# Performance work log

Hardware: AMD Instinct MI355X
Metric: run time of the kernel (lower is better)

The kernel has to match this reference:

```python
import jax, jax.numpy as jnp
import numpy as np

N = 40000; E = 640000; F_IN = 128; HID = 32; HEADS = 4; G = 64
NEG_SLOPE = 0.2; LN_EPS = 1e-5


def setup_inputs() -> dict:
    key = jax.random.key(0)
    ks = jax.random.split(key, 24)
    rn = lambda k, shape, s=0.1: jax.random.normal(k, shape, jnp.float32) * s
    d = {}
    d["x"] = jax.random.normal(ks[0], (N, F_IN), jnp.float32)
    d["edge_index"] = jax.random.randint(ks[1], (2, E), 0, N)
    d["batch"] = jnp.sort(jax.random.randint(ks[2], (N,), 0, G))
    # GAT layer 0: in F_IN -> HID per head, HEADS heads, concat
    d["W0"] = rn(ks[3], (F_IN, HEADS * HID))
    d["as0"] = rn(ks[4], (HEADS, HID)); d["ad0"] = rn(ks[5], (HEADS, HID))
    d["b0"] = jnp.zeros((HEADS * HID,), jnp.float32)
    d["ln0_g"] = jnp.ones((HEADS * HID,), jnp.float32); d["ln0_b"] = jnp.zeros((HEADS * HID,), jnp.float32)
    # GAT layer 1: HEADS*HID -> HID per head, HEADS heads, concat
    d["W1"] = rn(ks[6], (HEADS * HID, HEADS * HID))
    d["as1"] = rn(ks[7], (HEADS, HID)); d["ad1"] = rn(ks[8], (HEADS, HID))
    d["b1"] = jnp.zeros((HEADS * HID,), jnp.float32)
    d["ln1_g"] = jnp.ones((HEADS * HID,), jnp.float32); d["ln1_b"] = jnp.zeros((HEADS * HID,), jnp.float32)
    # GAT layer 2: HEADS*HID -> HID, 1 head, no concat
    d["W2"] = rn(ks[9], (HEADS * HID, HID))
    d["as2"] = rn(ks[10], (1, HID)); d["ad2"] = rn(ks[11], (1, HID))
    d["b2"] = jnp.zeros((HID,), jnp.float32)
    d["ln2_g"] = jnp.ones((HID,), jnp.float32); d["ln2_b"] = jnp.zeros((HID,), jnp.float32)
    # classifier: HID -> HID//2 -> 2
    d["fc1_w"] = rn(ks[12], (HID, HID // 2)); d["fc1_b"] = jnp.zeros((HID // 2,), jnp.float32)
    d["fc2_w"] = rn(ks[13], (HID // 2, 2)); d["fc2_b"] = jnp.zeros((2,), jnp.float32)
    return d


def gat_layer(x, src, dst, W, a_s, a_d, b, heads, out_c, concat):
    n = x.shape[0]
    h = (x @ W).reshape(n, heads, out_c)            # [N,H,C]
    al_s = jnp.sum(h * a_s, axis=-1)                # [N,H]
    al_d = jnp.sum(h * a_d, axis=-1)                # [N,H]
    e = jax.nn.leaky_relu(al_s[src] + al_d[dst], NEG_SLOPE)  # [E,H]
    m = jax.ops.segment_max(e, dst, num_segments=n)          # segment softmax over dst
    ex = jnp.exp(e - m[dst])
    s = jax.ops.segment_sum(ex, dst, num_segments=n)
    alpha = ex / (s[dst] + 1e-16)                   # [E,H]
    out = jax.ops.segment_sum(h[src] * alpha[:, :, None], dst, num_segments=n)  # [N,H,C]
    out = out.reshape(n, heads * out_c) if concat else out.mean(axis=1)
    return out + b


def layer_norm(x, g, b):
    mu = x.mean(-1, keepdims=True)
    var = jnp.var(x, axis=-1, keepdims=True)
    return (x - mu) * jax.lax.rsqrt(var + LN_EPS) * g + b


def reference(x, edge_index, batch, W0, as0, ad0, b0, ln0_g, ln0_b, W1, as1, ad1, b1, ln1_g, ln1_b, W2, as2, ad2, b2, ln2_g, ln2_b, fc1_w, fc1_b, fc2_w, fc2_b):
    src, dst = edge_index[0], edge_index[1]
    h = gat_layer(x, src, dst, W0, as0, ad0, b0, HEADS, HID, True)
    h = jax.nn.elu(layer_norm(h, ln0_g, ln0_b))
    h = gat_layer(h, src, dst, W1, as1, ad1, b1, HEADS, HID, True)
    h = jax.nn.elu(layer_norm(h, ln1_g, ln1_b))
    h = gat_layer(h, src, dst, W2, as2, ad2, b2, 1, HID, False)
    h = jax.nn.elu(layer_norm(h, ln2_g, ln2_b))
    cnt = jax.ops.segment_sum(jnp.ones((h.shape[0],), h.dtype), batch, num_segments=G)
    hg = jax.ops.segment_sum(h, batch, num_segments=G) / jnp.maximum(cnt, 1.0)[:, None]  # global mean pool [G,HID]
    z = jax.nn.relu(hg @ fc1_w + fc1_b)
    return z @ fc2_w + fc2_b
```

## Files before the change

kernel.cpp:

```cpp
#include <hip/hip_runtime.h>
#include <hip/hip_fp16.h>
#include <math.h>

#define NN 40000
#define EE 640000
#define NG 64
#define SCAN_BLOCKS ((NN + 1023) / 1024)

__device__ __forceinline__ float eluf(float x) { return x > 0.f ? x : expm1f(x); }

typedef const __attribute__((address_space(1))) char gas_char;
typedef __attribute__((address_space(3))) char las_char;

__device__ __forceinline__ void async_copy16(void* l, const void* g) {
  __builtin_amdgcn_global_load_lds((gas_char*)g, (las_char*)l, 16, 0, 0);
}

typedef __fp16 f16x2 __attribute__((ext_vector_type(2)));
__device__ __forceinline__ unsigned packh(float lo, float hi) {
  f16x2 p = __builtin_amdgcn_cvt_pkrtz(lo, hi);
  union { f16x2 h; unsigned u; } c; c.h = p; return c.u;
}
__device__ __forceinline__ float hlo(unsigned p) {
  union { unsigned u; f16x2 h; } c; c.u = p; return (float)c.h.x;
}
__device__ __forceinline__ float hhi(unsigned p) {
  union { unsigned u; f16x2 h; } c; c.u = p; return (float)c.h.y;
}
__device__ __forceinline__ float h16f(unsigned short u) {
  union { unsigned u32; f16x2 h; } c; c.u32 = u; return (float)c.h.x;
}

__global__ void zero_int_kernel(int* __restrict__ p, int n) {
  int i = blockIdx.x * 256 + threadIdx.x;
  if (i < n) p[i] = 0;
}

__global__ void count_deg_kernel(const int* __restrict__ dst, int* __restrict__ deg, int e) {
  int i0 = (blockIdx.x * 256 + threadIdx.x) * 4;
  if (i0 + 4 <= e) {
    int4 d4 = *reinterpret_cast<const int4*>(&dst[i0]);
    atomicAdd(&deg[d4.x], 1);
    atomicAdd(&deg[d4.y], 1);
    atomicAdd(&deg[d4.z], 1);
    atomicAdd(&deg[d4.w], 1);
  } else {
    for (int i = i0; i < e; ++i) atomicAdd(&deg[dst[i]], 1);
  }
}

__global__ __launch_bounds__(1024) void scanA_kernel(const int* __restrict__ deg,
                                                     int* __restrict__ row_ptr,
                                                     int* __restrict__ bsum, int n) {
  __shared__ int wsum[16];
  int t = threadIdx.x, lane = t & 63, wid = t >> 6;
  int i = blockIdx.x * 1024 + t;
  int v = (i < n) ? deg[i] : 0;
#pragma unroll
  for (int off = 1; off < 64; off <<= 1) {
    int u = __shfl_up(v, off);
    if (lane >= off) v += u;
  }
  if (lane == 63) wsum[wid] = v;
  __syncthreads();
  if (t < 16) {
    int w = wsum[t];
#pragma unroll
    for (int off = 1; off < 16; off <<= 1) {
      int u = __shfl_up(w, off);
      if (t >= off) w += u;
    }
    wsum[t] = w;
  }
  __syncthreads();
  if (wid > 0) v += wsum[wid - 1];
  if (i < n) row_ptr[i + 1] = v;
  if (t == 1023) bsum[blockIdx.x] = v;
}

__global__ __launch_bounds__(1024) void scanC_kernel(int* __restrict__ row_ptr,
                                                     const int* __restrict__ bsum,
                                                     int* __restrict__ cursor, int n) {
  __shared__ int off_s;
  int t = threadIdx.x;
  int b = blockIdx.x;
  if (t < 64) {
    int v = (t < b && t < SCAN_BLOCKS) ? bsum[t] : 0;
#pragma unroll
    for (int m = 1; m < 64; m <<= 1) v += __shfl_xor(v, m);
    if (t == 0) off_s = v;
  }
  __syncthreads();
  int off = off_s;
  int i = b * 1024 + t;
  if (i < n) {
    int v = row_ptr[i + 1] + off;
    row_ptr[i + 1] = v;
    if (i + 1 < n) cursor[i + 1] = v;
    if (i == 0) { cursor[0] = 0; row_ptr[0] = 0; }
  }
}

__global__ void scatter_kernel(const int* __restrict__ src, const int* __restrict__ dst,
                               int* __restrict__ cursor, int* __restrict__ csr_src, int e) {
  int i0 = (blockIdx.x * 256 + threadIdx.x) * 4;
  if (i0 + 4 <= e) {
    int4 s4 = *reinterpret_cast<const int4*>(&src[i0]);
    int4 d4 = *reinterpret_cast<const int4*>(&dst[i0]);
    int p0 = atomicAdd(&cursor[d4.x], 1);
    int p1 = atomicAdd(&cursor[d4.y], 1);
    int p2 = atomicAdd(&cursor[d4.z], 1);
    int p3 = atomicAdd(&cursor[d4.w], 1);
    csr_src[p0] = s4.x;
    csr_src[p1] = s4.y;
    csr_src[p2] = s4.z;
    csr_src[p3] = s4.w;
  } else {
    for (int i = i0; i < e; ++i) {
      int d = dst[i];
      int pos = atomicAdd(&cursor[d], 1);
      csr_src[pos] = src[i];
    }
  }
}

__global__ __launch_bounds__(256, 3) void gemm128_kernel(
    const float* __restrict__ x, const float* __restrict__ W,
    const float* __restrict__ a_s, const float* __restrict__ a_d,
    unsigned* __restrict__ hb, float* __restrict__ als, float* __restrict__ ald)
{
  __shared__ float xs[2][64 * 32];
  __shared__ float ws[2][32 * 128];

  int t = threadIdx.x;
  int row0 = blockIdx.x * 64;
  const char* xgb = (const char*)x + (size_t)row0 * 512;

  {
    int li0 = t, li1 = t + 256;
    async_copy16((char*)xs[0] + li0 * 16, xgb + (li0 >> 3) * 512 + (li0 & 7) * 16);
    async_copy16((char*)xs[0] + li1 * 16, xgb + (li1 >> 3) * 512 + (li1 & 7) * 16);
    const char* wg = (const char*)W;
#pragma unroll
    for (int p = 0; p < 4; ++p)
      async_copy16((char*)ws[0] + p * 4096 + t * 16, wg + p * 4096 + t * 16);
  }
  __syncthreads();

  int cg = t & 31, rg = t >> 5;
  int r0 = rg * 8;
  int jlo = 2 * cg;

  float acc[8][4];
#pragma unroll
  for (int r = 0; r < 8; ++r)
#pragma unroll
    for (int c = 0; c < 4; ++c) acc[r][c] = 0.f;

  for (int ch = 0; ch < 4; ++ch) {
    if (ch < 3) {
      int b = (ch + 1) & 1;
      int li0 = t, li1 = t + 256;
      const char* xg = xgb + (ch + 1) * 128;
      async_copy16((char*)xs[b] + li0 * 16, xg + (li0 >> 3) * 512 + (li0 & 7) * 16);
      async_copy16((char*)xs[b] + li1 * 16, xg + (li1 >> 3) * 512 + (li1 & 7) * 16);
      const char* wg = (const char*)W + (size_t)(ch + 1) * 32 * 128 * 4;
#pragma unroll
      for (int p = 0; p < 4; ++p)
        async_copy16((char*)ws[b] + p * 4096 + t * 16, wg + p * 4096 + t * 16);
    }
    const float* wc = ws[ch & 1];
    const float* xc = xs[ch & 1];
#pragma unroll
    for (int kk = 0; kk < 32; kk += 4) {
      float2 wlo[4], whi[4];
#pragma unroll
      for (int q = 0; q < 4; ++q) {
        wlo[q] = *reinterpret_cast<const float2*>(&wc[(kk + q) * 128 + jlo]);
        whi[q] = *reinterpret_cast<const float2*>(&wc[(kk + q) * 128 + 64 + jlo]);
      }
#pragma unroll
      for (int r = 0; r < 8; ++r) {
        float4 xv = *reinterpret_cast<const float4*>(&xc[(r0 + r) * 32 + kk]);
        float a0 = acc[r][0], a1 = acc[r][1], a2 = acc[r][2], a3 = acc[r][3];
        a0 = fmaf(xv.x, wlo[0].x, a0); a1 = fmaf(xv.x, wlo[0].y, a1);
        a2 = fmaf(xv.x, whi[0].x, a2); a3 = fmaf(xv.x, whi[0].y, a3);
        a0 = fmaf(xv.y, wlo[1].x, a0); a1 = fmaf(xv.y, wlo[1].y, a1);
        a2 = fmaf(xv.y, whi[1].x, a2); a3 = fmaf(xv.y, whi[1].y, a3);
        a0 = fmaf(xv.z, wlo[2].x, a0); a1 = fmaf(xv.z, wlo[2].y, a1);
        a2 = fmaf(xv.z, whi[2].x, a2); a3 = fmaf(xv.z, whi[2].y, a3);
        a0 = fmaf(xv.w, wlo[3].x, a0); a1 = fmaf(xv.w, wlo[3].y, a1);
        a2 = fmaf(xv.w, whi[3].x, a2); a3 = fmaf(xv.w, whi[3].y, a3);
        acc[r][0] = a0; acc[r][1] = a1; acc[r][2] = a2; acc[r][3] = a3;
      }
    }
    __syncthreads();
  }

#pragma unroll
  for (int r = 0; r < 8; ++r) {
    uint2 pv;
    pv.x = packh(acc[r][0], acc[r][2]);
    pv.y = packh(acc[r][1], acc[r][3]);
    *reinterpret_cast<uint2*>(&hb[(size_t)(row0 + r0 + r) * 64 + jlo]) = pv;
  }

  float as0 = a_s[jlo], as1 = a_s[jlo + 1], as2 = a_s[jlo + 64], as3 = a_s[jlo + 65];
  float ad0 = a_d[jlo], ad1 = a_d[jlo + 1], ad2 = a_d[jlo + 64], ad3 = a_d[jlo + 65];
  int lane = t & 63;
#pragma unroll
  for (int r = 0; r < 8; ++r) {
    float psa = fmaf(acc[r][0], as0, acc[r][1] * as1);
    float psb = fmaf(acc[r][2], as2, acc[r][3] * as3);
    float pda = fmaf(acc[r][0], ad0, acc[r][1] * ad1);
    float pdb = fmaf(acc[r][2], ad2, acc[r][3] * ad3);
#pragma unroll
    for (int m = 1; m < 16; m <<= 1) {
      psa += __shfl_xor(psa, m); psb += __shfl_xor(psb, m);
      pda += __shfl_xor(pda, m); pdb += __shfl_xor(pdb, m);
    }
    if ((lane & 15) == 0) {
      int hA = (lane >> 4) & 1;
      size_t row = (size_t)(row0 + r0 + r);
      als[row * 4 + hA] = psa; als[row * 4 + hA + 2] = psb;
      ald[row * 4 + hA] = pda; ald[row * 4 + hA + 2] = pdb;
    }
  }
}

template<bool FUSE>
__global__ __launch_bounds__(256) void aggregate128_kernel(
    const unsigned* __restrict__ hb, const float* __restrict__ als, const float* __restrict__ ald,
    const int* __restrict__ row_ptr, const int* __restrict__ csr_src,
    const float* __restrict__ bias, const float* __restrict__ ln_g, const float* __restrict__ ln_b,
    float* __restrict__ out,
    const float* __restrict__ W2, const float* __restrict__ as2, const float* __restrict__ ad2,
    unsigned short* __restrict__ h2h, float* __restrict__ als2, float* __restrict__ ald2)
{
  __shared__ int s_src[4][2][32];
  __shared__ float2 s_w[4][2][32][2];
  __shared__ __align__(16) float w2s[FUSE ? 32 * 128 : 4];
  __shared__ __align__(16) float y_s[FUSE ? 8 * 128 : 4];

  int t = threadIdx.x, lane = t & 63, wid = t >> 6;
  int hw = lane >> 5, c = lane & 31;
  int node = blockIdx.x * 8 + wid * 2 + hw;

  if constexpr (FUSE) {
#pragma unroll
    for (int p = 0; p < 4; ++p)
      async_copy16((char*)w2s + p * 4096 + t * 16, (const char*)W2 + p * 4096 + t * 16);
    __syncthreads();
  }

  int start = row_ptr[node], end = row_ptr[node + 1];
  int deg = end - start;

  float4 adq = reinterpret_cast<const float4*>(ald)[node];
  int hsel = c >> 4;
  float a0 = 0.f, a1 = 0.f, a2 = 0.f, a3 = 0.f;
  float ssum0 = 0.f, ssum1 = 0.f;

  if (deg <= 32) {
    int s = 0;
    float ex0 = 0.f, ex1 = 0.f, ex2 = 0.f, ex3 = 0.f;
    if (c < deg) {
      s = csr_src[start + c];
      float4 q = reinterpret_cast<const float4*>(als)[s];
      float v0 = q.x + adq.x, v1 = q.y + adq.y, v2 = q.z + adq.z, v3 = q.w + adq.w;
      v0 = v0 > 0.f ? v0 : 0.2f * v0; v1 = v1 > 0.f ? v1 : 0.2f * v1;
      v2 = v2 > 0.f ? v2 : 0.2f * v2; v3 = v3 > 0.f ? v3 : 0.2f * v3;
      ex0 = __expf(v0); ex1 = __expf(v1); ex2 = __expf(v2); ex3 = __expf(v3);
    }
    s_src[wid][hw][c] = s;
    s_w[wid][hw][c][0] = make_float2(ex0, ex2);
    s_w[wid][hw][c][1] = make_float2(ex1, ex3);

    float b0a = 0.f, b1a = 0.f, b2a = 0.f, b3a = 0.f;
    float sb0 = 0.f, sb1 = 0.f;
    int j = 0;
    for (; j + 2 <= deg; j += 2) {
      int sa = s_src[wid][hw][j];
      int sb = s_src[wid][hw][j + 1];
      uint2 ua = *reinterpret_cast<const uint2*>(&hb[(size_t)sa * 64 + 2 * c]);
      uint2 ub = *reinterpret_cast<const uint2*>(&hb[(size_t)sb * 64 + 2 * c]);
      float2 wa = s_w[wid][hw][j][hsel];
      float2 wb = s_w[wid][hw][j + 1][hsel];
      a0 = fmaf(wa.x, hlo(ua.x), a0); a1 = fmaf(wa.x, hlo(ua.y), a1);
      a2 = fmaf(wa.y, hhi(ua.x), a2); a3 = fmaf(wa.y, hhi(ua.y), a3);
      ssum0 += wa.x; ssum1 += wa.y;
      b0a = fmaf(wb.x, hlo(ub.x), b0a); b1a = fmaf(wb.x, hlo(ub.y), b1a);
      b2a = fmaf(wb.y, hhi(ub.x), b2a); b3a = fmaf(wb.y, hhi(ub.y), b3a);
      sb0 += wb.x; sb1 += wb.y;
    }
    if (j < deg) {
      int sa = s_src[wid][hw][j];
      uint2 ua = *reinterpret_cast<const uint2*>(&hb[(size_t)sa * 64 + 2 * c]);
      float2 wa = s_w[wid][hw][j][hsel];
      a0 = fmaf(wa.x, hlo(ua.x), a0); a1 = fmaf(wa.x, hlo(ua.y), a1);
      a2 = fmaf(wa.y, hhi(ua.x), a2); a3 = fmaf(wa.y, hhi(ua.y), a3);
      ssum0 += wa.x; ssum1 += wa.y;
    }
    a0 += b0a; a1 += b1a; a2 += b2a; a3 += b3a;
    ssum0 += sb0; ssum1 += sb1;
  } else {
    for (int eb = 0; eb < deg; eb += 32) {
      int s = 0;
      float ex0 = 0.f, ex1 = 0.f, ex2 = 0.f, ex3 = 0.f;
      if (eb + c < deg) {
        s = csr_src[start + eb + c];
        float4 q = reinterpret_cast<const float4*>(als)[s];
        float v0 = q.x + adq.x, v1 = q.y + adq.y, v2 = q.z + adq.z, v3 = q.w + adq.w;
        v0 = v0 > 0.f ? v0 : 0.2f * v0; v1 = v1 > 0.f ? v1 : 0.2f * v1;
        v2 = v2 > 0.f ? v2 : 0.2f * v2; v3 = v3 > 0.f ? v3 : 0.2f * v3;
        ex0 = __expf(v0); ex1 = __expf(v1); ex2 = __expf(v2); ex3 = __expf(v3);
      }
      s_src[wid][hw][c] = s;
      s_w[wid][hw][c][0] = make_float2(ex0, ex2);
      s_w[wid][hw][c][1] = make_float2(ex1, ex3);
      int cnt = deg - eb; if (cnt > 32) cnt = 32;
      for (int j = 0; j < cnt; ++j) {
        int sj = s_src[wid][hw][j];
        uint2 u = *reinterpret_cast<const uint2*>(&hb[(size_t)sj * 64 + 2 * c]);
        float2 w = s_w[wid][hw][j][hsel];
        a0 = fmaf(w.x, hlo(u.x), a0); a1 = fmaf(w.x, hlo(u.y), a1);
        a2 = fmaf(w.y, hhi(u.x), a2); a3 = fmaf(w.y, hhi(u.y), a3);
        ssum0 += w.x; ssum1 += w.y;
      }
    }
  }

  float2 blo = *reinterpret_cast<const float2*>(&bias[2 * c]);
  float2 bhi = *reinterpret_cast<const float2*>(&bias[2 * c + 64]);
  float is0 = 1.f / (ssum0 + 1e-16f), is1 = 1.f / (ssum1 + 1e-16f);
  float o0 = a0 * is0 + blo.x;
  float o1 = a1 * is0 + blo.y;
  float o2 = a2 * is1 + bhi.x;
  float o3 = a3 * is1 + bhi.y;
  float red = o0 + o1 + o2 + o3;
  float sq2 = o0 * o0 + o1 * o1 + o2 * o2 + o3 * o3;
#pragma unroll
  for (int m = 1; m < 32; m <<= 1) {
    red += __shfl_xor(red, m);
    sq2 += __shfl_xor(sq2, m);
  }
  float mu = red * (1.f / 128.f);
  float var = sq2 * (1.f / 128.f) - mu * mu;
  float rstd = rsqrtf(var + 1e-5f);
  float2 glo = *reinterpret_cast<const float2*>(&ln_g[2 * c]);
  float2 ghi = *reinterpret_cast<const float2*>(&ln_g[2 * c + 64]);
  float2 bl2 = *reinterpret_cast<const float2*>(&ln_b[2 * c]);
  float2 bh2 = *reinterpret_cast<const float2*>(&ln_b[2 * c + 64]);
  float2 ylo, yhi;
  ylo.x = eluf((o0 - mu) * rstd * glo.x + bl2.x);
  ylo.y = eluf((o1 - mu) * rstd * glo.y + bl2.y);
  yhi.x = eluf((o2 - mu) * rstd * ghi.x + bh2.x);
  yhi.y = eluf((o3 - mu) * rstd * ghi.y + bh2.y);

  if constexpr (!FUSE) {
    *reinterpret_cast<float2*>(&out[(size_t)node * 128 + 2 * c]) = ylo;
    *reinterpret_cast<float2*>(&out[(size_t)node * 128 + 64 + 2 * c]) = yhi;
  } else {
    int nidx = (wid * 2 + hw) * 128;
    *reinterpret_cast<float2*>(&y_s[nidx + 2 * c]) = ylo;
    *reinterpret_cast<float2*>(&y_s[nidx + 64 + 2 * c]) = yhi;
    float ac0 = 0.f, ac1 = 0.f, ac2 = 0.f, ac3 = 0.f;
#pragma unroll
    for (int k = 0; k < 128; k += 4) {
      float4 yv = *reinterpret_cast<const float4*>(&y_s[nidx + k]);
      ac0 = fmaf(yv.x, w2s[(k + 0) * 32 + c], ac0);
      ac1 = fmaf(yv.y, w2s[(k + 1) * 32 + c], ac1);
      ac2 = fmaf(yv.z, w2s[(k + 2) * 32 + c], ac2);
      ac3 = fmaf(yv.w, w2s[(k + 3) * 32 + c], ac3);
    }
    float acc = (ac0 + ac1) + (ac2 + ac3);
    h2h[(size_t)node * 32 + c] = (unsigned short)(packh(acc, acc) & 0xffffu);
    float ps = acc * as2[c], pd = acc * ad2[c];
#pragma unroll
    for (int m = 1; m < 32; m <<= 1) { ps += __shfl_xor(ps, m); pd += __shfl_xor(pd, m); }
    if (c == 0) { als2[node] = ps; ald2[node] = pd; }
  }
}

__global__ __launch_bounds__(256) void aggregate32_kernel(
    const unsigned short* __restrict__ h, const float* __restrict__ als, const float* __restrict__ ald,
    const int* __restrict__ row_ptr, const int* __restrict__ csr_src,
    const float* __restrict__ bias, const float* __restrict__ ln_g, const float* __restrict__ ln_b,
    float* __restrict__ out, int n)
{
  __shared__ int s_src[4][2][32];
  __shared__ float s_ex[4][2][32];
  int t = threadIdx.x, lane = t & 63, wid = t >> 6;
  int hw = lane >> 5, c = lane & 31;
  int node = blockIdx.x * 8 + wid * 2 + hw;
  int start = row_ptr[node], end = row_ptr[node + 1];
  int deg = end - start;
  float adl = ald[node];
  float acc0 = 0.f, ssum = 0.f;

  if (deg <= 32) {
    int s = 0; float ex = 0.f;
    if (c < deg) {
      s = csr_src[start + c];
      float v = als[s] + adl;
      v = v > 0.f ? v : 0.2f * v;
      ex = __expf(v);
    }
    s_src[wid][hw][c] = s;
    s_ex[wid][hw][c] = ex;

    float acc1 = 0.f, ssum1 = 0.f;
    int j = 0;
    for (; j + 2 <= deg; j += 2) {
      int sa = s_src[wid][hw][j];
      int sb = s_src[wid][hw][j + 1];
      float ha = h16f(h[(size_t)sa * 32 + c]);
      float hbv = h16f(h[(size_t)sb * 32 + c]);
      float wa = s_ex[wid][hw][j];
      float wb = s_ex[wid][hw][j + 1];
      acc0 = fmaf(wa, ha, acc0); ssum += wa;
      acc1 = fmaf(wb, hbv, acc1); ssum1 += wb;
    }
    if (j < deg) {
      float wa = s_ex[wid][hw][j];
      acc0 = fmaf(wa, h16f(h[(size_t)s_src[wid][hw][j] * 32 + c]), acc0);
      ssum += wa;
    }
    acc0 += acc1; ssum += ssum1;
  } else {
    for (int eb = 0; eb < deg; eb += 32) {
      int s = 0; float ex = 0.f;
      if (eb + c < deg) {
        s = csr_src[start + eb + c];
        float v = als[s] + adl;
        v = v > 0.f ? v : 0.2f * v;
        ex = __expf(v);
      }
      s_src[wid][hw][c] = s;
      s_ex[wid][hw][c] = ex;
      int cnt = deg - eb; if (cnt > 32) cnt = 32;
      for (int j = 0; j < cnt; ++j) {
        float w = s_ex[wid][hw][j];
        acc0 = fmaf(w, h16f(h[(size_t)s_src[wid][hw][j] * 32 + c]), acc0);
        ssum += w;
      }
    }
  }

  float o0 = acc0 / (ssum + 1e-16f) + bias[c];
  float red = o0, sq2 = o0 * o0;
#pragma unroll
  for (int m = 1; m < 32; m <<= 1) {
    red += __shfl_xor(red, m);
    sq2 += __shfl_xor(sq2, m);
  }
  float mu = red * (1.f / 32.f);
  float var = sq2 * (1.f / 32.f) - mu * mu;
  float rstd = rsqrtf(var + 1e-5f);
  float y0 = (o0 - mu) * rstd * ln_g[c] + ln_b[c];
  out[(size_t)node * 32 + c] = eluf(y0);
}

__device__ __forceinline__ int lower_bound_dev(const int* a, int n, int key) {
  int lo = 0, hi = n;
  while (lo < hi) { int mid = (lo + hi) >> 1; if (a[mid] < key) lo = mid + 1; else hi = mid; }
  return lo;
}

__global__ __launch_bounds__(256) void poolfc_kernel(
    const float* __restrict__ x2, const int* __restrict__ batch,
    const float* __restrict__ fc1w, const float* __restrict__ fc1b,
    const float* __restrict__ fc2w, const float* __restrict__ fc2b,
    float* __restrict__ out, int n)
{
  int g = blockIdx.x;
  int lo = lower_bound_dev(batch, n, g);
  int hi = lower_bound_dev(batch, n, g + 1);
  int t = threadIdx.x;
  int c = t & 31, r = t >> 5;
  float acc = 0.f;
  for (int i = lo + r; i < hi; i += 8) acc += x2[(size_t)i * 32 + c];
  __shared__ float red[8][32];
  __shared__ float hgl[32];
  __shared__ float zl[16];
  red[r][c] = acc;
  __syncthreads();
  if (r == 0) {
    float s = 0.f;
#pragma unroll
    for (int k = 0; k < 8; ++k) s += red[k][c];
    float cnt = (float)(hi - lo);
    hgl[c] = s / fmaxf(cnt, 1.f);
  }
  __syncthreads();
  if (t < 16) {
    float a = fc1b[t];
#pragma unroll
    for (int k = 0; k < 32; ++k) a = fmaf(hgl[k], fc1w[k * 16 + t], a);
    zl[t] = fmaxf(a, 0.f);
  }
  __syncthreads();
  if (t < 2) {
    float a = fc2b[t];
#pragma unroll
    for (int j = 0; j < 16; ++j) a = fmaf(zl[j], fc2w[j * 2 + t], a);
    out[g * 2 + t] = a;
  }
}

extern "C" void kernel_launch(void* const* d_in, const int* in_sizes, int n_in,
                              void* d_out, int out_size, void* d_ws, size_t ws_size,
                              hipStream_t stream) {
  const float* x    = (const float*)d_in[0];
  const int*   ei   = (const int*)d_in[1];
  const int*   batch= (const int*)d_in[2];
  const float* W0   = (const float*)d_in[3];
  const float* as0  = (const float*)d_in[4];
  const float* ad0  = (const float*)d_in[5];
  const float* b0   = (const float*)d_in[6];
  const float* ln0g = (const float*)d_in[7];
  const float* ln0b = (const float*)d_in[8];
  const float* W1   = (const float*)d_in[9];
  const float* as1  = (const float*)d_in[10];
  const float* ad1  = (const float*)d_in[11];
  const float* b1   = (const float*)d_in[12];
  const float* ln1g = (const float*)d_in[13];
  const float* ln1b = (const float*)d_in[14];
  const float* W2   = (const float*)d_in[15];
  const float* as2  = (const float*)d_in[16];
  const float* ad2  = (const float*)d_in[17];
  const float* b2   = (const float*)d_in[18];
  const float* ln2g = (const float*)d_in[19];
  const float* ln2b = (const float*)d_in[20];
  const float* fc1w = (const float*)d_in[21];
  const float* fc1b = (const float*)d_in[22];
  const float* fc2w = (const float*)d_in[23];
  const float* fc2b = (const float*)d_in[24];
  float* out = (float*)d_out;

  const int* srce = ei;
  const int* dste = ei + EE;

  unsigned* hb = (unsigned*)d_ws;
  float* B2  = (float*)(hb + (size_t)NN * 64);
  float* als = B2 + (size_t)NN * 128;
  float* ald = als + (size_t)NN * 4;
  unsigned short* h2h = (unsigned short*)(ald + (size_t)NN * 4);
  float* x2  = (float*)(h2h + (size_t)NN * 32);
  float* als2 = x2 + (size_t)NN * 32;
  float* ald2 = als2 + NN;
  int* deg      = (int*)(ald2 + NN);
  int* row_ptr  = deg + NN;
  int* cursor   = row_ptr + NN + 1;
  int* csr_src  = cursor + NN;
  int* bsum     = csr_src + EE;

  zero_int_kernel<<<(NN + 255) / 256, 256, 0, stream>>>(deg, NN);
  count_deg_kernel<<<(EE / 4 + 255) / 256, 256, 0, stream>>>(dste, deg, EE);
  scanA_kernel<<<SCAN_BLOCKS, 1024, 0, stream>>>(deg, row_ptr, bsum, NN);
  scanC_kernel<<<SCAN_BLOCKS, 1024, 0, stream>>>(row_ptr, bsum, cursor, NN);
  scatter_kernel<<<(EE / 4 + 255) / 256, 256, 0, stream>>>(srce, dste, cursor, csr_src, EE);

  gemm128_kernel<<<625, 256, 0, stream>>>(x, W0, as0, ad0, hb, als, ald);
  aggregate128_kernel<false><<<NN / 8, 256, 0, stream>>>(hb, als, ald, row_ptr, csr_src,
                                                         b0, ln0g, ln0b, B2,
                                                         nullptr, nullptr, nullptr,
                                                         nullptr, nullptr, nullptr);
  gemm128_kernel<<<625, 256, 0, stream>>>(B2, W1, as1, ad1, hb, als, ald);
  aggregate128_kernel<true><<<NN / 8, 256, 0, stream>>>(hb, als, ald, row_ptr, csr_src,
                                                        b1, ln1g, ln1b, nullptr,
                                                        W2, as2, ad2, h2h, als2, ald2);
  aggregate32_kernel<<<NN / 8, 256, 0, stream>>>(h2h, als2, ald2, row_ptr, csr_src,
                                                 b2, ln2g, ln2b, x2, NN);
  poolfc_kernel<<<NG, 256, 0, stream>>>(x2, batch, fc1w, fc1b, fc2w, fc2b, out, NN);
}
```

Before: 254.6 us.

## Use 16 lanes per node with wider gathers in GAT aggregation kernels

```diff
diff --git a/kernel.cpp b/kernel.cpp
--- a/kernel.cpp
+++ b/kernel.cpp
@@ -26,9 +26,6 @@
 }
 __device__ __forceinline__ float hhi(unsigned p) {
   union { unsigned u; f16x2 h; } c; c.u = p; return (float)c.h.y;
-}
-__device__ __forceinline__ float h16f(unsigned short u) {
-  union { unsigned u32; f16x2 h; } c; c.u32 = u; return (float)c.h.x;
 }
 
 __global__ void zero_int_kernel(int* __restrict__ p, int n) {
@@ -237,14 +234,14 @@
     const float* __restrict__ W2, const float* __restrict__ as2, const float* __restrict__ ad2,
     unsigned short* __restrict__ h2h, float* __restrict__ als2, float* __restrict__ ald2)
 {
-  __shared__ int s_src[4][2][32];
-  __shared__ float2 s_w[4][2][32][2];
+  __shared__ int s_src[4][4][17];
+  __shared__ float2 s_w[4][4][17][2];
   __shared__ __align__(16) float w2s[FUSE ? 32 * 128 : 4];
-  __shared__ __align__(16) float y_s[FUSE ? 8 * 128 : 4];
+  __shared__ __align__(16) float y_s[FUSE ? 16 * 132 : 4];
 
   int t = threadIdx.x, lane = t & 63, wid = t >> 6;
-  int hw = lane >> 5, c = lane & 31;
-  int node = blockIdx.x * 8 + wid * 2 + hw;
+  int q = lane >> 4, c4 = lane & 15;
+  int node = blockIdx.x * 16 + wid * 4 + q;
 
   if constexpr (FUSE) {
 #pragma unroll
@@ -257,128 +254,121 @@
   int deg = end - start;
 
   float4 adq = reinterpret_cast<const float4*>(ald)[node];
-  int hsel = c >> 4;
+  int hsel = c4 >> 3;
+  const uint4* hbase = reinterpret_cast<const uint4*>(hb + 4 * c4);
   float a0 = 0.f, a1 = 0.f, a2 = 0.f, a3 = 0.f;
-  float ssum0 = 0.f, ssum1 = 0.f;
-
-  if (deg <= 32) {
+  float a4 = 0.f, a5 = 0.f, a6 = 0.f, a7 = 0.f;
+  float b0 = 0.f, b1 = 0.f, b2 = 0.f, b3 = 0.f;
+  float b4 = 0.f, b5 = 0.f, b6 = 0.f, b7 = 0.f;
+  float ssum0 = 0.f, ssum1 = 0.f, sb0 = 0.f, sb1 = 0.f;
+
+  for (int eb = 0; eb < deg; eb += 16) {
     int s = 0;
     float ex0 = 0.f, ex1 = 0.f, ex2 = 0.f, ex3 = 0.f;
-    if (c < deg) {
-      s = csr_src[start + c];
-      float4 q = reinterpret_cast<const float4*>(als)[s];
-      float v0 = q.x + adq.x, v1 = q.y + adq.y, v2 = q.z + adq.z, v3 = q.w + adq.w;
+    if (eb + c4 < deg) {
+      s = csr_src[start + eb + c4];
+      float4 qv = reinterpret_cast<const float4*>(als)[s];
+      float v0 = qv.x + adq.x, v1 = qv.y + adq.y, v2 = qv.z + adq.z, v3 = qv.w + adq.w;
       v0 = v0 > 0.f ? v0 : 0.2f * v0; v1 = v1 > 0.f ? v1 : 0.2f * v1;
       v2 = v2 > 0.f ? v2 : 0.2f * v2; v3 = v3 > 0.f ? v3 : 0.2f * v3;
       ex0 = __expf(v0); ex1 = __expf(v1); ex2 = __expf(v2); ex3 = __expf(v3);
     }
-    s_src[wid][hw][c] = s;
-    s_w[wid][hw][c][0] = make_float2(ex0, ex2);
-    s_w[wid][hw][c][1] = make_float2(ex1, ex3);
-
-    float b0a = 0.f, b1a = 0.f, b2a = 0.f, b3a = 0.f;
-    float sb0 = 0.f, sb1 = 0.f;
+    s_src[wid][q][c4] = s;
+    s_w[wid][q][c4][0] = make_float2(ex0, ex2);
+    s_w[wid][q][c4][1] = make_float2(ex1, ex3);
+
+    int cnt = deg - eb; if (cnt > 16) cnt = 16;
     int j = 0;
-    for (; j + 2 <= deg; j += 2) {
-      int sa = s_src[wid][hw][j];
-      int sb = s_src[wid][hw][j + 1];
-      uint2 ua = *reinterpret_cast<const uint2*>(&hb[(size_t)sa * 64 + 2 * c]);
-      uint2 ub = *reinterpret_cast<const uint2*>(&hb[(size_t)sb * 64 + 2 * c]);
-      float2 wa = s_w[wid][hw][j][hsel];
-      float2 wb = s_w[wid][hw][j + 1][hsel];
+    for (; j + 2 <= cnt; j += 2) {
+      int sa = s_src[wid][q][j];
+      int sb = s_src[wid][q][j + 1];
+      uint4 ua = hbase[(size_t)sa * 16];
+      uint4 ub = hbase[(size_t)sb * 16];
+      float2 wa = s_w[wid][q][j][hsel];
+      float2 wb = s_w[wid][q][j + 1][hsel];
       a0 = fmaf(wa.x, hlo(ua.x), a0); a1 = fmaf(wa.x, hlo(ua.y), a1);
-      a2 = fmaf(wa.y, hhi(ua.x), a2); a3 = fmaf(wa.y, hhi(ua.y), a3);
+      a2 = fmaf(wa.x, hlo(ua.z), a2); a3 = fmaf(wa.x, hlo(ua.w), a3);
+      a4 = fmaf(wa.y, hhi(ua.x), a4); a5 = fmaf(wa.y, hhi(ua.y), a5);
+      a6 = fmaf(wa.y, hhi(ua.z), a6); a7 = fmaf(wa.y, hhi(ua.w), a7);
       ssum0 += wa.x; ssum1 += wa.y;
-      b0a = fmaf(wb.x, hlo(ub.x), b0a); b1a = fmaf(wb.x, hlo(ub.y), b1a);
-      b2a = fmaf(wb.y, hhi(ub.x), b2a); b3a = fmaf(wb.y, hhi(ub.y), b3a);
+      b0 = fmaf(wb.x, hlo(ub.x), b0); b1 = fmaf(wb.x, hlo(ub.y), b1);
+      b2 = fmaf(wb.x, hlo(ub.z), b2); b3 = fmaf(wb.x, hlo(ub.w), b3);
+      b4 = fmaf(wb.y, hhi(ub.x), b4); b5 = fmaf(wb.y, hhi(ub.y), b5);
+      b6 = fmaf(wb.y, hhi(ub.z), b6); b7 = fmaf(wb.y, hhi(ub.w), b7);
       sb0 += wb.x; sb1 += wb.y;
     }
-    if (j < deg) {
-      int sa = s_src[wid][hw][j];
-      uint2 ua = *reinterpret_cast<const uint2*>(&hb[(size_t)sa * 64 + 2 * c]);
-      float2 wa = s_w[wid][hw][j][hsel];
+    if (j < cnt) {
+      int sa = s_src[wid][q][j];
+      uint4 ua = hbase[(size_t)sa * 16];
+      float2 wa = s_w[wid][q][j][hsel];
       a0 = fmaf(wa.x, hlo(ua.x), a0); a1 = fmaf(wa.x, hlo(ua.y), a1);
-      a2 = fmaf(wa.y, hhi(ua.x), a2); a3 = fmaf(wa.y, hhi(ua.y), a3);
+      a2 = fmaf(wa.x, hlo(ua.z), a2); a3 = fmaf(wa.x, hlo(ua.w), a3);
+      a4 = fmaf(wa.y, hhi(ua.x), a4); a5 = fmaf(wa.y, hhi(ua.y), a5);
+      a6 = fmaf(wa.y, hhi(ua.z), a6); a7 = fmaf(wa.y, hhi(ua.w), a7);
       ssum0 += wa.x; ssum1 += wa.y;
     }
-    a0 += b0a; a1 += b1a; a2 += b2a; a3 += b3a;
-    ssum0 += sb0; ssum1 += sb1;
-  } else {
-    for (int eb = 0; eb < deg; eb += 32) {
-      int s = 0;
-      float ex0 = 0.f, ex1 = 0.f, ex2 = 0.f, ex3 = 0.f;
-      if (eb + c < deg) {
-        s = csr_src[start + eb + c];
-        float4 q = reinterpret_cast<const float4*>(als)[s];
-        float v0 = q.x + adq.x, v1 = q.y + adq.y, v2 = q.z + adq.z, v3 = q.w + adq.w;
-        v0 = v0 > 0.f ? v0 : 0.2f * v0; v1 = v1 > 0.f ? v1 : 0.2f * v1;
-        v2 = v2 > 0.f ? v2 : 0.2f * v2; v3 = v3 > 0.f ? v3 : 0.2f * v3;
-        ex0 = __expf(v0); ex1 = __expf(v1); ex2 = __expf(v2); ex3 = __expf(v3);
-      }
-      s_src[wid][hw][c] = s;
-      s_w[wid][hw][c][0] = make_float2(ex0, ex2);
-      s_w[wid][hw][c][1] = make_float2(ex1, ex3);
-      int cnt = deg - eb; if (cnt > 32) cnt = 32;
-      for (int j = 0; j < cnt; ++j) {
-        int sj = s_src[wid][hw][j];
-        uint2 u = *reinterpret_cast<const uint2*>(&hb[(size_t)sj * 64 + 2 * c]);
-        float2 w = s_w[wid][hw][j][hsel];
-        a0 = fmaf(w.x, hlo(u.x), a0); a1 = fmaf(w.x, hlo(u.y), a1);
-        a2 = fmaf(w.y, hhi(u.x), a2); a3 = fmaf(w.y, hhi(u.y), a3);
-        ssum0 += w.x; ssum1 += w.y;
-      }
-    }
-  }
-
-  float2 blo = *reinterpret_cast<const float2*>(&bias[2 * c]);
-  float2 bhi = *reinterpret_cast<const float2*>(&bias[2 * c + 64]);
+  }
+  a0 += b0; a1 += b1; a2 += b2; a3 += b3;
+  a4 += b4; a5 += b5; a6 += b6; a7 += b7;
+  ssum0 += sb0; ssum1 += sb1;
+
+  float4 blo = *reinterpret_cast<const float4*>(&bias[4 * c4]);
+  float4 bhi = *reinterpret_cast<const float4*>(&bias[64 + 4 * c4]);
   float is0 = 1.f / (ssum0 + 1e-16f), is1 = 1.f / (ssum1 + 1e-16f);
-  float o0 = a0 * is0 + blo.x;
-  float o1 = a1 * is0 + blo.y;
-  float o2 = a2 * is1 + bhi.x;
-  float o3 = a3 * is1 + bhi.y;
-  float red = o0 + o1 + o2 + o3;
-  float sq2 = o0 * o0 + o1 * o1 + o2 * o2 + o3 * o3;
-#pragma unroll
-  for (int m = 1; m < 32; m <<= 1) {
+  float o0 = a0 * is0 + blo.x, o1 = a1 * is0 + blo.y;
+  float o2 = a2 * is0 + blo.z, o3 = a3 * is0 + blo.w;
+  float o4 = a4 * is1 + bhi.x, o5 = a5 * is1 + bhi.y;
+  float o6 = a6 * is1 + bhi.z, o7 = a7 * is1 + bhi.w;
+  float red = (o0 + o1 + o2 + o3) + (o4 + o5 + o6 + o7);
+  float sq2 = (o0 * o0 + o1 * o1 + o2 * o2 + o3 * o3)
+            + (o4 * o4 + o5 * o5 + o6 * o6 + o7 * o7);
+#pragma unroll
+  for (int m = 1; m < 16; m <<= 1) {
     red += __shfl_xor(red, m);
     sq2 += __shfl_xor(sq2, m);
   }
   float mu = red * (1.f / 128.f);
   float var = sq2 * (1.f / 128.f) - mu * mu;
   float rstd = rsqrtf(var + 1e-5f);
-  float2 glo = *reinterpret_cast<const float2*>(&ln_g[2 * c]);
-  float2 ghi = *reinterpret_cast<const float2*>(&ln_g[2 * c + 64]);
-  float2 bl2 = *reinterpret_cast<const float2*>(&ln_b[2 * c]);
-  float2 bh2 = *reinterpret_cast<const float2*>(&ln_b[2 * c + 64]);
-  float2 ylo, yhi;
+  float4 glo = *reinterpret_cast<const float4*>(&ln_g[4 * c4]);
+  float4 ghi = *reinterpret_cast<const float4*>(&ln_g[64 + 4 * c4]);
+  float4 bl2 = *reinterpret_cast<const float4*>(&ln_b[4 * c4]);
+  float4 bh2 = *reinterpret_cast<const float4*>(&ln_b[64 + 4 * c4]);
+  float4 ylo, yhi;
   ylo.x = eluf((o0 - mu) * rstd * glo.x + bl2.x);
   ylo.y = eluf((o1 - mu) * rstd * glo.y + bl2.y);
-  yhi.x = eluf((o2 - mu) * rstd * ghi.x + bh2.x);
-  yhi.y = eluf((o3 - mu) * rstd * ghi.y + bh2.y);
+  ylo.z = eluf((o2 - mu) * rstd * glo.z + bl2.z);
+  ylo.w = eluf((o3 - mu) * rstd * glo.w + bl2.w);
+  yhi.x = eluf((o4 - mu) * rstd * ghi.x + bh2.x);
+  yhi.y = eluf((o5 - mu) * rstd * ghi.y + bh2.y);
+  yhi.z = eluf((o6 - mu) * rstd * ghi.z + bh2.z);
+  yhi.w = eluf((o7 - mu) * rstd * ghi.w + bh2.w);
 
   if constexpr (!FUSE) {
-    *reinterpret_cast<float2*>(&out[(size_t)node * 128 + 2 * c]) = ylo;
-    *reinterpret_cast<float2*>(&out[(size_t)node * 128 + 64 + 2 * c]) = yhi;
+    *reinterpret_cast<float4*>(&out[(size_t)node * 128 + 4 * c4]) = ylo;
+    *reinterpret_cast<float4*>(&out[(size_t)node * 128 + 64 + 4 * c4]) = yhi;
   } else {
-    int nidx = (wid * 2 + hw) * 128;
-    *reinterpret_cast<float2*>(&y_s[nidx + 2 * c]) = ylo;
-    *reinterpret_cast<float2*>(&y_s[nidx + 64 + 2 * c]) = yhi;
-    float ac0 = 0.f, ac1 = 0.f, ac2 = 0.f, ac3 = 0.f;
-#pragma unroll
-    for (int k = 0; k < 128; k += 4) {
-      float4 yv = *reinterpret_cast<const float4*>(&y_s[nidx + k]);
-      ac0 = fmaf(yv.x, w2s[(k + 0) * 32 + c], ac0);
-      ac1 = fmaf(yv.y, w2s[(k + 1) * 32 + c], ac1);
-      ac2 = fmaf(yv.z, w2s[(k + 2) * 32 + c], ac2);
-      ac3 = fmaf(yv.w, w2s[(k + 3) * 32 + c], ac3);
-    }
-    float acc = (ac0 + ac1) + (ac2 + ac3);
-    h2h[(size_t)node * 32 + c] = (unsigned short)(packh(acc, acc) & 0xffffu);
-    float ps = acc * as2[c], pd = acc * ad2[c];
-#pragma unroll
-    for (int m = 1; m < 32; m <<= 1) { ps += __shfl_xor(ps, m); pd += __shfl_xor(pd, m); }
-    if (c == 0) { als2[node] = ps; ald2[node] = pd; }
+    int nidx = (wid * 4 + q) * 132;
+    *reinterpret_cast<float4*>(&y_s[nidx + 4 * c4]) = ylo;
+    *reinterpret_cast<float4*>(&y_s[nidx + 64 + 4 * c4]) = yhi;
+    float d0 = 0.f, d1 = 0.f, d2 = 0.f, d3 = 0.f;
+#pragma unroll
+    for (int k = 0; k < 128; k += 2) {
+      float2 yv = *reinterpret_cast<const float2*>(&y_s[nidx + k]);
+      d0 = fmaf(yv.x, w2s[k * 32 + c4], d0);
+      d1 = fmaf(yv.y, w2s[(k + 1) * 32 + c4], d1);
+      d2 = fmaf(yv.x, w2s[k * 32 + c4 + 16], d2);
+      d3 = fmaf(yv.y, w2s[(k + 1) * 32 + c4 + 16], d3);
+    }
+    float accA = d0 + d1, accB = d2 + d3;
+    unsigned pa = packh(accA, accB);
+    h2h[(size_t)node * 32 + c4] = (unsigned short)(pa & 0xffffu);
+    h2h[(size_t)node * 32 + c4 + 16] = (unsigned short)(pa >> 16);
+    float ps = fmaf(accA, as2[c4], accB * as2[c4 + 16]);
+    float pd = fmaf(accA, ad2[c4], accB * ad2[c4 + 16]);
+#pragma unroll
+    for (int m = 1; m < 16; m <<= 1) { ps += __shfl_xor(ps, m); pd += __shfl_xor(pd, m); }
+    if (c4 == 0) { als2[node] = ps; ald2[node] = pd; }
   }
 }
 
@@ -388,77 +378,69 @@
     const float* __restrict__ bias, const float* __restrict__ ln_g, const float* __restrict__ ln_b,
     float* __restrict__ out, int n)
 {
-  __shared__ int s_src[4][2][32];
-  __shared__ float s_ex[4][2][32];
+  __shared__ int s_src[4][4][17];
+  __shared__ float s_ex[4][4][17];
   int t = threadIdx.x, lane = t & 63, wid = t >> 6;
-  int hw = lane >> 5, c = lane & 31;
-  int node = blockIdx.x * 8 + wid * 2 + hw;
+  int q = lane >> 4, c4 = lane & 15;
+  int node = blockIdx.x * 16 + wid * 4 + q;
   int start = row_ptr[node], end = row_ptr[node + 1];
   int deg = end - start;
   float adl = ald[node];
-  float acc0 = 0.f, ssum = 0.f;
-
-  if (deg <= 32) {
+  const unsigned* hu = reinterpret_cast<const unsigned*>(h);
+  float acc0 = 0.f, acc1 = 0.f, bc0 = 0.f, bc1 = 0.f;
+  float ssum = 0.f, sb = 0.f;
+
+  for (int eb = 0; eb < deg; eb += 16) {
     int s = 0; float ex = 0.f;
-    if (c < deg) {
-      s = csr_src[start + c];
+    if (eb + c4 < deg) {
+      s = csr_src[start + eb + c4];
       float v = als[s] + adl;
       v = v > 0.f ? v : 0.2f * v;
       ex = __expf(v);
     }
-    s_src[wid][hw][c] = s;
-    s_ex[wid][hw][c] = ex;
-
-    float acc1 = 0.f, ssum1 = 0.f;
+    s_src[wid][q][c4] = s;
+    s_ex[wid][q][c4] = ex;
+
+    int cnt = deg - eb; if (cnt > 16) cnt = 16;
     int j = 0;
-    for (; j + 2 <= deg; j += 2) {
-      int sa = s_src[wid][hw][j];
-      int sb = s_src[wid][hw][j + 1];
-      float ha = h16f(h[(size_t)sa * 32 + c]);
-      float hbv = h16f(h[(size_t)sb * 32 + c]);
-      float wa = s_ex[wid][hw][j];
-      float wb = s_ex[wid][hw][j + 1];
-      acc0 = fmaf(wa, ha, acc0); ssum += wa;
-      acc1 = fmaf(wb, hbv, acc1); ssum1 += wb;
-    }
-    if (j < deg) {
-      float wa = s_ex[wid][hw][j];
-      acc0 = fmaf(wa, h16f(h[(size_t)s_src[wid][hw][j] * 32 + c]), acc0);
-      ssum += wa;
-    }
-    acc0 += acc1; ssum += ssum1;
-  } else {
-    for (int eb = 0; eb < deg; eb += 32) {
-      int s = 0; float ex = 0.f;
-      if (eb + c < deg) {
-        s = csr_src[start + eb + c];
-        float v = als[s] + adl;
-        v = v > 0.f ? v : 0.2f * v;
-        ex = __expf(v);
-      }
-      s_src[wid][hw][c] = s;
-      s_ex[wid][hw][c] = ex;
-      int cnt = deg - eb; if (cnt > 32) cnt = 32;
-      for (int j = 0; j < cnt; ++j) {
-        float w = s_ex[wid][hw][j];
-        acc0 = fmaf(w, h16f(h[(size_t)s_src[wid][hw][j] * 32 + c]), acc0);
-        ssum += w;
-      }
-    }
-  }
-
-  float o0 = acc0 / (ssum + 1e-16f) + bias[c];
-  float red = o0, sq2 = o0 * o0;
-#pragma unroll
-  for (int m = 1; m < 32; m <<= 1) {
+    for (; j + 2 <= cnt; j += 2) {
+      int sa = s_src[wid][q][j];
+      int sbx = s_src[wid][q][j + 1];
+      unsigned ua = hu[(size_t)sa * 16 + c4];
+      unsigned ub = hu[(size_t)sbx * 16 + c4];
+      float wa = s_ex[wid][q][j];
+      float wb = s_ex[wid][q][j + 1];
+      acc0 = fmaf(wa, hlo(ua), acc0); acc1 = fmaf(wa, hhi(ua), acc1); ssum += wa;
+      bc0 = fmaf(wb, hlo(ub), bc0); bc1 = fmaf(wb, hhi(ub), bc1); sb += wb;
+    }
+    if (j < cnt) {
+      int sa = s_src[wid][q][j];
+      unsigned ua = hu[(size_t)sa * 16 + c4];
+      float wa = s_ex[wid][q][j];
+      acc0 = fmaf(wa, hlo(ua), acc0); acc1 = fmaf(wa, hhi(ua), acc1); ssum += wa;
+    }
+  }
+  acc0 += bc0; acc1 += bc1; ssum += sb;
+
+  float2 bv = *reinterpret_cast<const float2*>(&bias[2 * c4]);
+  float is = 1.f / (ssum + 1e-16f);
+  float o0 = acc0 * is + bv.x;
+  float o1 = acc1 * is + bv.y;
+  float red = o0 + o1, sq2 = o0 * o0 + o1 * o1;
+#pragma unroll
+  for (int m = 1; m < 16; m <<= 1) {
     red += __shfl_xor(red, m);
     sq2 += __shfl_xor(sq2, m);
   }
   float mu = red * (1.f / 32.f);
   float var = sq2 * (1.f / 32.f) - mu * mu;
   float rstd = rsqrtf(var + 1e-5f);
-  float y0 = (o0 - mu) * rstd * ln_g[c] + ln_b[c];
-  out[(size_t)node * 32 + c] = eluf(y0);
+  float2 gv = *reinterpret_cast<const float2*>(&ln_g[2 * c4]);
+  float2 lb = *reinterpret_cast<const float2*>(&ln_b[2 * c4]);
+  float2 yv;
+  yv.x = eluf((o0 - mu) * rstd * gv.x + lb.x);
+  yv.y = eluf((o1 - mu) * rstd * gv.y + lb.y);
+  *reinterpret_cast<float2*>(&out[(size_t)node * 32 + 2 * c4]) = yv;
 }
 
 __device__ __forceinline__ int lower_bound_dev(const int* a, int n, int key) {
@@ -562,15 +544,15 @@
   scatter_kernel<<<(EE / 4 + 255) / 256, 256, 0, stream>>>(srce, dste, cursor, csr_src, EE);
 
   gemm128_kernel<<<625, 256, 0, stream>>>(x, W0, as0, ad0, hb, als, ald);
-  aggregate128_kernel<false><<<NN / 8, 256, 0, stream>>>(hb, als, ald, row_ptr, csr_src,
-                                                         b0, ln0g, ln0b, B2,
-                                                         nullptr, nullptr, nullptr,
-                                                         nullptr, nullptr, nullptr);
+  aggregate128_kernel<false><<<NN / 16, 256, 0, stream>>>(hb, als, ald, row_ptr, csr_src,
+                                                          b0, ln0g, ln0b, B2,
+                                                          nullptr, nullptr, nullptr,
+                                                          nullptr, nullptr, nullptr);
   gemm128_kernel<<<625, 256, 0, stream>>>(B2, W1, as1, ad1, hb, als, ald);
-  aggregate128_kernel<true><<<NN / 8, 256, 0, stream>>>(hb, als, ald, row_ptr, csr_src,
-                                                        b1, ln1g, ln1b, nullptr,
-                                                        W2, as2, ad2, h2h, als2, ald2);
-  aggregate32_kernel<<<NN / 8, 256, 0, stream>>>(h2h, als2, ald2, row_ptr, csr_src,
-                                                 b2, ln2g, ln2b, x2, NN);
+  aggregate128_kernel<true><<<NN / 16, 256, 0, stream>>>(hb, als, ald, row_ptr, csr_src,
+                                                         b1, ln1g, ln1b, nullptr,
+                                                         W2, as2, ad2, h2h, als2, ald2);
+  aggregate32_kernel<<<NN / 16, 256, 0, stream>>>(h2h, als2, ald2, row_ptr, csr_src,
+                                                  b2, ln2g, ln2b, x2, NN);
   poolfc_kernel<<<NG, 256, 0, stream>>>(x2, batch, fc1w, fc1b, fc2w, fc2b, out, NN);
 }
```

Result: faster. 244.9 us (-3.8%).
